# Optimization experiments

Measured on AMD Instinct MI355X. Metric: run time of the kernel, lower is better.

The kernel has to match this reference:

```python
import jax, jax.numpy as jnp
import numpy as np

N_HEADS = 16
LATENT = 16          # latent_vec_len (1D RoPE portion of head_dim)
ROPE_BASE = 10000.0
HIDDEN = 1024


def _rope_1d_tables(seq_len, d):
    m = d // 2
    inv_freq = 1.0 / (ROPE_BASE ** (jnp.arange(m, dtype=jnp.float32) * 2.0 / d))
    ang = jnp.arange(seq_len, dtype=jnp.float32)[:, None] * inv_freq[None, :]  # (S, m)
    return jnp.cos(ang), jnp.sin(ang)


def _rope_2d_tables(height, width, d):
    m = d // 4
    inv_freq = 1.0 / (ROPE_BASE ** (jnp.arange(m, dtype=jnp.float32) * 4.0 / d))
    xa = jnp.arange(width, dtype=jnp.float32)[:, None] * inv_freq[None, :]   # (W, m)
    ya = jnp.arange(height, dtype=jnp.float32)[:, None] * inv_freq[None, :]  # (H, m)
    S = height * width
    cos_x = jnp.broadcast_to(jnp.cos(xa)[None, :, :], (height, width, m)).reshape(S, m)
    sin_x = jnp.broadcast_to(jnp.sin(xa)[None, :, :], (height, width, m)).reshape(S, m)
    cos_y = jnp.broadcast_to(jnp.cos(ya)[:, None, :], (height, width, m)).reshape(S, m)
    sin_y = jnp.broadcast_to(jnp.sin(ya)[:, None, :], (height, width, m)).reshape(S, m)
    return cos_x, sin_x, cos_y, sin_y


def _apply_rope_1d(x, cos, sin):
    # x: (B, n, S, d) with d even; cos/sin: (S, d//2)
    d = x.shape[-1]
    xr = x.reshape(*x.shape[:-1], d // 2, 2)
    a, b = xr[..., 0], xr[..., 1]
    na = a * cos - b * sin
    nb = a * sin + b * cos
    return jnp.stack((na, nb), axis=-1).reshape(x.shape)


def _apply_rope_2d(x, cos_x, sin_x, cos_y, sin_y):
    # x: (B, n, S, d) with d % 4 == 0; tables: (S, d//4)
    q = x.shape[-1] // 4
    xr, xi = x[..., :q], x[..., q:2 * q]
    yr, yi = x[..., 2 * q:3 * q], x[..., 3 * q:]
    return jnp.concatenate([
        xr * cos_x - xi * sin_x,
        xr * sin_x + xi * cos_x,
        yr * cos_y - yi * sin_y,
        yr * sin_y + yi * cos_y,
    ], axis=-1)


def setup_inputs() -> dict:
    key = jax.random.key(0)
    ks = jax.random.split(key, 9)
    B, S, D = 16, 1024, HIDDEN
    s = 1.0 / np.sqrt(D)
    inp = {
        'x': jax.random.normal(ks[0], (B, S, D), dtype=jnp.float32),
        'Wq': jax.random.uniform(ks[1], (D, D), jnp.float32, -s, s),
        'bq': jax.random.uniform(ks[2], (D,), jnp.float32, -s, s),
        'Wk': jax.random.uniform(ks[3], (D, D), jnp.float32, -s, s),
        'bk': jax.random.uniform(ks[4], (D,), jnp.float32, -s, s),
        'Wv': jax.random.uniform(ks[5], (D, D), jnp.float32, -s, s),
        'bv': jax.random.uniform(ks[6], (D,), jnp.float32, -s, s),
        'Wo': jax.random.uniform(ks[7], (D, D), jnp.float32, -s, s),
        'bo': jax.random.uniform(ks[8], (D,), jnp.float32, -s, s),
        'height': 32,
        'width': 32,
    }
    return inp


def reference(x, Wq, bq, Wk, bk, Wv, bv, Wo, bo, height, width):
    B, S, D = x.shape
    n, h = N_HEADS, D // N_HEADS
    spatial = h - LATENT
    scale = 1.0 / np.sqrt(h)

    def heads(t):
        return t.reshape(B, S, n, h).transpose(0, 2, 1, 3)  # (B, n, S, h)

    q = heads(x @ Wq.T + bq)
    k = heads(x @ Wk.T + bk)
    v = heads(x @ Wv.T + bv)

    cos1, sin1 = _rope_1d_tables(S, LATENT)
    cx, sx, cy, sy = _rope_2d_tables(height, width, spatial)

    ql = _apply_rope_1d(q[..., :LATENT], cos1, sin1)
    kl = _apply_rope_1d(k[..., :LATENT], cos1, sin1)
    qs = _apply_rope_2d(q[..., LATENT:], cx, sx, cy, sy)
    ks_ = _apply_rope_2d(k[..., LATENT:], cx, sx, cy, sy)

    qr = jnp.concatenate([ql, qs], axis=-1)
    kr = jnp.concatenate([kl, ks_], axis=-1)

    attn = jax.nn.softmax(jnp.einsum('bnsh,bnth->bnst', qr, kr) * scale, axis=-1)
    out = jnp.einsum('bnst,bnth->bnsh', attn, v)
    out = out.transpose(0, 2, 1, 3).reshape(B, S, D)
    return out @ Wo.T + bo
```

## Files before the change

### kernel.cpp

```cpp
#include <hip/hip_runtime.h>
#include <math.h>

#define B_ 16
#define S_ 1024
#define D_ 1024
#define NH_ 16
#define M_TOT (B_ * S_)

typedef __attribute__((ext_vector_type(8))) short short8v;
typedef __attribute__((ext_vector_type(4))) short short4v;
typedef __attribute__((ext_vector_type(4))) float float4v;
typedef __attribute__((ext_vector_type(4))) unsigned int uint4v;

static __device__ __forceinline__ unsigned short f2bf(float f) {
  union { float f; unsigned u; } x; x.f = f;
  unsigned r = (x.u + 0x7fffu + ((x.u >> 16) & 1u)) >> 16;
  return (unsigned short)r;
}
static __device__ __forceinline__ float bf2f(unsigned short u) {
  union { unsigned u; float f; } x; x.u = ((unsigned)u) << 16;
  return x.f;
}

static __device__ __forceinline__ unsigned pack2bf(float a, float b) {
  return ((unsigned)f2bf(b) << 16) | (unsigned)f2bf(a);
}

static __device__ __forceinline__ void load_lds16(const unsigned short* g, unsigned short* l) {
  __builtin_amdgcn_global_load_lds(
      (const __attribute__((address_space(1))) unsigned int*)g,
      (__attribute__((address_space(3))) unsigned int*)l, 16, 0, 0);
}

__global__ __launch_bounds__(256) void prep(
    const float* __restrict__ x, unsigned short* __restrict__ xb,
    const float* __restrict__ w0, const float* __restrict__ w1,
    const float* __restrict__ w2, const float* __restrict__ w3,
    unsigned short* __restrict__ wdst,
    float* __restrict__ cos1, float* __restrict__ sin1,
    float* __restrict__ cos2, float* __restrict__ sin2) {
  const int bid = blockIdx.x;
  if (bid < 16384) {
    int i = bid * 256 + threadIdx.x;
    float4 v = ((const float4*)x)[i];
    unsigned short tt[4] = {f2bf(v.x), f2bf(v.y), f2bf(v.z), f2bf(v.w)};
    ((short4v*)xb)[i] = *(short4v*)tt;
  } else if (bid < 20480) {
    int wi = (bid - 16384) * 256 + threadIdx.x;
    int m = wi >> 18;
    int i = wi & 262143;
    const float* src = (m == 0) ? w0 : (m == 1) ? w1 : (m == 2) ? w2 : w3;
    float4 v = ((const float4*)src)[i];
    unsigned short tt[4] = {f2bf(v.x), f2bf(v.y), f2bf(v.z), f2bf(v.w)};
    ((short4v*)(wdst + (size_t)m * D_ * D_))[i] = *(short4v*)tt;
  } else {
    int t = (bid - 20480) * 256 + threadIdx.x;
    if (t < S_ * 8) {
      int s = t >> 3, i = t & 7;
      double ang = (double)s * pow(10000.0, -(double)i / 8.0);
      cos1[t] = (float)cos(ang);
      sin1[t] = (float)sin(ang);
    } else if (t < S_ * 8 + 384) {
      int u = t - S_ * 8;
      int p = u / 12, j = u - p * 12;
      double ang = (double)p * pow(10000.0, -(double)j / 12.0);
      cos2[u] = (float)cos(ang);
      sin2[u] = (float)sin(ang);
    }
  }
}

template <bool BF16OUT>
__global__ __launch_bounds__(256) void gemm_mfma(
    const unsigned short* __restrict__ A, const unsigned short* __restrict__ Wall,
    const float* __restrict__ b0, const float* __restrict__ b1,
    const float* __restrict__ b2, void* __restrict__ Cout) {
  __shared__ unsigned short As[2][128 * 32];
  __shared__ unsigned short Bs[2][128 * 32];
  const int y = blockIdx.y;
  const unsigned short* W = Wall + (size_t)y * D_ * D_;
  const float* bias = (y == 0) ? b0 : (y == 1) ? b1 : b2;
  const int t = threadIdx.x;
  const int w = t >> 6, L = t & 63;
  const int c = L & 15, g = L >> 4;
  const int id = blockIdx.x;
  const int xcd = id & 7, slot = id >> 3;
  const int bn = (slot & 7) * 128;
  const int bm = ((slot >> 3) * 8 + xcd) * 128;

  const int srow = w * 32 + (L >> 2);
  const int sko = (L & 3) * 8;
  const unsigned short* gA = A + (size_t)(bm + srow) * D_ + sko;
  const unsigned short* gB = W + (size_t)(bn + srow) * D_ + sko;

  const int wm = (w >> 1) * 64, wn = (w & 1) * 64;

  float4v acc[4][4];
#pragma unroll
  for (int i = 0; i < 4; ++i)
#pragma unroll
    for (int j = 0; j < 4; ++j) acc[i][j] = (float4v){0.f, 0.f, 0.f, 0.f};

#define GS(buf, k0_)                                                  \
  {                                                                   \
    load_lds16(gA + (k0_), &As[buf][w * 1024]);                       \
    load_lds16(gA + (k0_) + 16 * D_, &As[buf][w * 1024 + 512]);       \
    load_lds16(gB + (k0_), &Bs[buf][w * 1024]);                       \
    load_lds16(gB + (k0_) + 16 * D_, &Bs[buf][w * 1024 + 512]);       \
  }

  GS(0, 0);
  asm volatile("s_waitcnt vmcnt(0)" ::: "memory");
  __syncthreads();
  int cur = 0;
  for (int k0 = 0; k0 < D_; k0 += 32) {
    if (k0 + 32 < D_) GS(cur ^ 1, k0 + 32);
    short8v af[4], bf[4];
#pragma unroll
    for (int i = 0; i < 4; ++i)
      af[i] = *(const short8v*)&As[cur][(wm + 16 * i + c) * 32 + 8 * g];
#pragma unroll
    for (int j = 0; j < 4; ++j)
      bf[j] = *(const short8v*)&Bs[cur][(wn + 16 * j + c) * 32 + 8 * g];
#pragma unroll
    for (int i = 0; i < 4; ++i)
#pragma unroll
      for (int j = 0; j < 4; ++j)
        acc[i][j] = __builtin_amdgcn_mfma_f32_16x16x32_bf16(af[i], bf[j], acc[i][j], 0, 0, 0);
    asm volatile("s_waitcnt vmcnt(0)" ::: "memory");
    __syncthreads();
    cur ^= 1;
  }
#undef GS
  unsigned short* Cb = (unsigned short*)Cout + (size_t)y * M_TOT * D_;
#pragma unroll
  for (int i = 0; i < 4; ++i)
#pragma unroll
    for (int r = 0; r < 4; ++r) {
      const size_t row = (size_t)bm + wm + 16 * i + 4 * g + r;
#pragma unroll
      for (int j = 0; j < 4; ++j) {
        const int col = bn + wn + 16 * j + c;
        float vv = acc[i][j][r] + bias[col];
        if (BF16OUT)
          Cb[row * D_ + col] = f2bf(vv);
        else
          ((float*)Cout)[row * D_ + col] = vv;
      }
    }
}

__global__ __launch_bounds__(256) void postproc(
    unsigned short* __restrict__ qb, unsigned short* __restrict__ kbuf,
    const unsigned short* __restrict__ vb, unsigned short* __restrict__ vT,
    const float* __restrict__ cos1, const float* __restrict__ sin1,
    const float* __restrict__ cos2, const float* __restrict__ sin2) {
  __shared__ unsigned short T[64][72];
  const int bid = blockIdx.x;
  if (bid < 65536) {
    unsigned short* q = (bid < 32768) ? qb : kbuf;
    const float scale = (bid < 32768) ? 0.125f : 1.0f;
    int tid = (bid & 32767) * 256 + threadIdx.x;
    int u = tid & 511;
    int m = tid >> 9;
    int s = m & (S_ - 1);
    int head = u >> 5, w = u & 31;
    size_t base = (size_t)m * D_ + head * 64;
    size_t c0, c1;
    float cv, sv;
    if (w < 8) {
      c0 = base + 2 * w; c1 = c0 + 1;
      cv = cos1[s * 8 + w]; sv = sin1[s * 8 + w];
    } else if (w < 20) {
      int j = w - 8, x = s & 31;
      c0 = base + 16 + j; c1 = base + 28 + j;
      cv = cos2[x * 12 + j]; sv = sin2[x * 12 + j];
    } else {
      int j = w - 20, yy = s >> 5;
      c0 = base + 40 + j; c1 = base + 52 + j;
      cv = cos2[yy * 12 + j]; sv = sin2[yy * 12 + j];
    }
    float a = bf2f(q[c0]), b = bf2f(q[c1]);
    q[c0] = f2bf((a * cv - b * sv) * scale);
    q[c1] = f2bf((a * sv + b * cv) * scale);
  } else {
    const int tb = bid - 65536;
    const int t = threadIdx.x;
    const int st0 = (tb & 15) * 64;
    const int hd = (tb >> 4) & 15, b = tb >> 8;
    const unsigned short* src = vb + ((size_t)b * S_ + st0) * D_ + hd * 64;
#pragma unroll
    for (int rep = 0; rep < 4; ++rep) {
      int id = t + rep * 256;
      int s = id >> 4, n4 = (id & 15) * 4;
      short4v val = *(const short4v*)(src + (size_t)s * D_ + n4);
      T[n4 + 0][s] = val[0]; T[n4 + 1][s] = val[1];
      T[n4 + 2][s] = val[2]; T[n4 + 3][s] = val[3];
    }
    __syncthreads();
    unsigned short* dst = vT + ((size_t)(b * NH_ + hd) * 64) * S_ + st0;
#pragma unroll
    for (int rep = 0; rep < 2; ++rep) {
      int id = t + rep * 256;
      int n = id >> 3, s8 = (id & 7) * 8;
      unsigned short tmp[8];
#pragma unroll
      for (int u2 = 0; u2 < 8; ++u2) tmp[u2] = T[n][s8 + u2];
      *(short8v*)(dst + (size_t)n * S_ + s8) = *(short8v*)tmp;
    }
  }
}

__global__ __launch_bounds__(256, 4) void attn_mfma(
    const unsigned short* __restrict__ qb, const unsigned short* __restrict__ kb,
    const unsigned short* __restrict__ vT, unsigned short* __restrict__ out) {
  __shared__ unsigned short KV[2][2][4096];
  const int t = threadIdx.x;
  const int w = t >> 6;
  const int L = t & 63;
  const int c = L & 15;
  const int g = L >> 4;
  const int id = blockIdx.x;
  const int xcd = id & 7, slot = id >> 3;
  const int qt = slot & 7;
  const int pair = (slot >> 3) * 8 + xcd;
  const int b = pair >> 4, hd = pair & 15;
  const size_t mrow0 = (size_t)b * S_ + qt * 128 + w * 32;
  const int dcol0 = hd * 64;

  const int lrow = L >> 3;
  const int lcol = ((L & 7) ^ lrow) * 8;

  const int a_lo = (((L & 16) ? 32 : 0) + c) * 4;
  const int a_hi = a_lo + 64;
  const bool ghi = (L >= 32);
  const int swz = (c & 7) << 3;

  short8v aq[2][2];
#pragma unroll
  for (int i = 0; i < 2; ++i)
#pragma unroll
    for (int st = 0; st < 2; ++st)
      aq[i][st] = *(const short8v*)(qb + (mrow0 + 16 * i + c) * D_ + dcol0 + 32 * st + 8 * g);

  float4v oacc[2][4];
  float lsum[2] = {0.f, 0.f};
#pragma unroll
  for (int i = 0; i < 2; ++i)
#pragma unroll
    for (int jv = 0; jv < 4; ++jv) oacc[i][jv] = (float4v){0.f, 0.f, 0.f, 0.f};

  const unsigned short* vbase = vT + (size_t)(b * NH_ + hd) * 64 * S_;
  const unsigned short* kbb = kb + (size_t)b * S_ * D_ + dcol0;

#define STAGE(buf, kt_)                                                          \
  {                                                                              \
    _Pragma("unroll")                                                            \
    for (int e = 0; e < 2; ++e) {                                                \
      const int seg = 2 * w + e;                                                 \
      const int row = seg * 8 + lrow;                                            \
      load_lds16(kbb + (size_t)((kt_) * 64 + row) * D_ + lcol,                   \
                 &KV[buf][0][seg * 512]);                                        \
      load_lds16(vbase + (size_t)row * S_ + (kt_) * 64 + lcol,                   \
                 &KV[buf][1][seg * 512]);                                        \
    }                                                                            \
  }

  STAGE(0, 0);
  asm volatile("s_waitcnt vmcnt(0)" ::: "memory");
  __syncthreads();

#pragma unroll 1
  for (int kt = 0; kt < 16; ++kt) {
    const int cur = kt & 1;
    if (kt < 15) STAGE(cur ^ 1, kt + 1);
#pragma unroll
    for (int st = 0; st < 2; ++st) {
      short8v vfh[4];
#pragma unroll
      for (int jv = 0; jv < 4; ++jv)
        vfh[jv] = *(const short8v*)&KV[cur][1][((16 * jv + c) * 64 + st * 32 + 8 * g) ^ swz];
      short8v kfh[2][2];
#pragma unroll
      for (int jl = 0; jl < 2; ++jl)
#pragma unroll
        for (int h = 0; h < 2; ++h)
          kfh[jl][h] = *(const short8v*)&KV[cur][0][((16 * (2 * st + jl) + c) * 64 + h * 32 + 8 * g) ^ swz];
      float4v sacch[2][2];
#pragma unroll
      for (int i = 0; i < 2; ++i)
#pragma unroll
        for (int jl = 0; jl < 2; ++jl) sacch[i][jl] = (float4v){0.f, 0.f, 0.f, 0.f};
      __builtin_amdgcn_s_setprio(1);
#pragma unroll
      for (int jl = 0; jl < 2; ++jl)
#pragma unroll
        for (int i = 0; i < 2; ++i) {
          sacch[i][jl] = __builtin_amdgcn_mfma_f32_16x16x32_bf16(kfh[jl][0], aq[i][0], sacch[i][jl], 0, 0, 0);
          sacch[i][jl] = __builtin_amdgcn_mfma_f32_16x16x32_bf16(kfh[jl][1], aq[i][1], sacch[i][jl], 0, 0, 0);
        }
      __builtin_amdgcn_s_setprio(0);
      unsigned pkh[2][2][2];
#pragma unroll
      for (int i = 0; i < 2; ++i)
#pragma unroll
        for (int jl = 0; jl < 2; ++jl) {
          float p0 = __expf(sacch[i][jl][0]);
          float p1 = __expf(sacch[i][jl][1]);
          float p2 = __expf(sacch[i][jl][2]);
          float p3 = __expf(sacch[i][jl][3]);
          lsum[i] += (p0 + p1) + (p2 + p3);
          pkh[i][jl][0] = pack2bf(p0, p1);
          pkh[i][jl][1] = pack2bf(p2, p3);
        }
      short8v aph[2];
#pragma unroll
      for (int i = 0; i < 2; ++i) {
        uint4v wv;
#pragma unroll
        for (int q2 = 0; q2 < 4; ++q2) {
          const int addr = (q2 & 2) ? a_hi : a_lo;
          int vlo = __builtin_amdgcn_ds_bpermute(addr, (int)pkh[i][0][q2 & 1]);
          int vhi = __builtin_amdgcn_ds_bpermute(addr, (int)pkh[i][1][q2 & 1]);
          wv[q2] = (unsigned)(ghi ? vhi : vlo);
        }
        aph[i] = *(short8v*)&wv;
      }
      __builtin_amdgcn_s_setprio(1);
#pragma unroll
      for (int jv = 0; jv < 4; ++jv)
#pragma unroll
        for (int i = 0; i < 2; ++i)
          oacc[i][jv] = __builtin_amdgcn_mfma_f32_16x16x32_bf16(aph[i], vfh[jv], oacc[i][jv], 0, 0, 0);
      __builtin_amdgcn_s_setprio(0);
    }
    asm volatile("s_waitcnt vmcnt(0)" ::: "memory");
    __syncthreads();
  }
#undef STAGE
#pragma unroll
  for (int i = 0; i < 2; ++i) {
    float ls = lsum[i];
    ls += __shfl_xor(ls, 16);
    ls += __shfl_xor(ls, 32);
#pragma unroll
    for (int r = 0; r < 4; ++r) {
      float inv = 1.f / __shfl(ls, 4 * g + r);
      size_t row = mrow0 + 16 * i + 4 * g + r;
#pragma unroll
      for (int jv = 0; jv < 4; ++jv)
        out[row * D_ + dcol0 + 16 * jv + c] = f2bf(oacc[i][jv][r] * inv);
    }
  }
}

extern "C" void kernel_launch(void* const* d_in, const int* in_sizes, int n_in,
                              void* d_out, int out_size, void* d_ws, size_t ws_size,
                              hipStream_t stream) {
  const float* x  = (const float*)d_in[0];
  const float* Wq = (const float*)d_in[1];
  const float* bq = (const float*)d_in[2];
  const float* Wk = (const float*)d_in[3];
  const float* bk = (const float*)d_in[4];
  const float* Wv = (const float*)d_in[5];
  const float* bv = (const float*)d_in[6];
  const float* Wo = (const float*)d_in[7];
  const float* bo = (const float*)d_in[8];
  float* out = (float*)d_out;

  char* ws = (char*)d_ws;
  const size_t SZ2 = (size_t)M_TOT * D_ * 2;
  unsigned short* xb = (unsigned short*)(ws);
  unsigned short* ob = xb;
  unsigned short* qb = (unsigned short*)(ws + SZ2);
  unsigned short* kb = (unsigned short*)(ws + 2 * SZ2);
  unsigned short* vb = (unsigned short*)(ws + 3 * SZ2);
  unsigned short* vT = (unsigned short*)(ws + 4 * SZ2);
  unsigned short* wqb = (unsigned short*)(ws + 5 * SZ2);
  unsigned short* wob = wqb + 3 * (size_t)D_ * D_;
  float* cos1 = (float*)(ws + 5 * SZ2 + 4 * (size_t)D_ * D_ * 2);
  float* sin1 = cos1 + S_ * 8;
  float* cos2 = sin1 + S_ * 8;
  float* sin2 = cos2 + 384;

  prep<<<20514, 256, 0, stream>>>(x, xb, Wq, Wk, Wv, Wo, wqb,
                                  cos1, sin1, cos2, sin2);
  gemm_mfma<true><<<dim3(1024, 3), 256, 0, stream>>>(xb, wqb, bq, bk, bv, qb);
  postproc<<<69632, 256, 0, stream>>>(qb, kb, vb, vT, cos1, sin1, cos2, sin2);
  attn_mfma<<<2048, 256, 0, stream>>>(qb, kb, vT, ob);
  gemm_mfma<false><<<dim3(1024, 1), 256, 0, stream>>>(ob, wob, bo, bo, bo, out);
}
```

Baseline: 485.4 us.

## Triple-buffer GEMM LDS tiles with partial vmcnt waits and single barrier

Switches the projection GEMM from double to triple-buffered LDS staging. Each step waits only for the older tile's loads (vmcnt(4)) and issues one raw s_barrier before prefetching two tiles ahead. The aim is to keep global-to-LDS loads in flight across MFMA compute instead of draining every iteration. It costs 50% more LDS per block, which may reduce occupancy, and the hand-counted wait/barrier ordering must be correct to avoid races.

After: 466.7 us. 3.8% less time.

```diff
diff --git a/kernel.cpp b/kernel.cpp
--- a/kernel.cpp
+++ b/kernel.cpp
@@ -75,8 +75,8 @@
     const unsigned short* __restrict__ A, const unsigned short* __restrict__ Wall,
     const float* __restrict__ b0, const float* __restrict__ b1,
     const float* __restrict__ b2, void* __restrict__ Cout) {
-  __shared__ unsigned short As[2][128 * 32];
-  __shared__ unsigned short Bs[2][128 * 32];
+  __shared__ unsigned short As[3][128 * 32];
+  __shared__ unsigned short Bs[3][128 * 32];
   const int y = blockIdx.y;
   const unsigned short* W = Wall + (size_t)y * D_ * D_;
   const float* bias = (y == 0) ? b0 : (y == 1) ? b1 : b2;
@@ -101,37 +101,48 @@
 #pragma unroll
     for (int j = 0; j < 4; ++j) acc[i][j] = (float4v){0.f, 0.f, 0.f, 0.f};
 
-#define GS(buf, k0_)                                                  \
-  {                                                                   \
-    load_lds16(gA + (k0_), &As[buf][w * 1024]);                       \
-    load_lds16(gA + (k0_) + 16 * D_, &As[buf][w * 1024 + 512]);       \
-    load_lds16(gB + (k0_), &Bs[buf][w * 1024]);                       \
-    load_lds16(gB + (k0_) + 16 * D_, &Bs[buf][w * 1024 + 512]);       \
+#define GS(buf, kt_)                                                   \
+  {                                                                    \
+    load_lds16(gA + (kt_) * 32, &As[buf][w * 1024]);                   \
+    load_lds16(gA + (kt_) * 32 + 16 * D_, &As[buf][w * 1024 + 512]);   \
+    load_lds16(gB + (kt_) * 32, &Bs[buf][w * 1024]);                   \
+    load_lds16(gB + (kt_) * 32 + 16 * D_, &Bs[buf][w * 1024 + 512]);   \
+  }
+#define VWAIT4 asm volatile("s_waitcnt vmcnt(4)" ::: "memory")
+#define VWAIT0 asm volatile("s_waitcnt vmcnt(0)" ::: "memory")
+#define BARRIER asm volatile("s_barrier" ::: "memory")
+#define COMPUTE(cur)                                                     \
+  {                                                                      \
+    short8v af[4], bf[4];                                                \
+    _Pragma("unroll")                                                    \
+    for (int i = 0; i < 4; ++i)                                          \
+      af[i] = *(const short8v*)&As[cur][(wm + 16 * i + c) * 32 + 8 * g]; \
+    _Pragma("unroll")                                                    \
+    for (int j = 0; j < 4; ++j)                                          \
+      bf[j] = *(const short8v*)&Bs[cur][(wn + 16 * j + c) * 32 + 8 * g]; \
+    _Pragma("unroll")                                                    \
+    for (int i = 0; i < 4; ++i)                                          \
+      _Pragma("unroll")                                                  \
+      for (int j = 0; j < 4; ++j)                                        \
+        acc[i][j] = __builtin_amdgcn_mfma_f32_16x16x32_bf16(             \
+            af[i], bf[j], acc[i][j], 0, 0, 0);                           \
   }
 
   GS(0, 0);
-  asm volatile("s_waitcnt vmcnt(0)" ::: "memory");
-  __syncthreads();
-  int cur = 0;
-  for (int k0 = 0; k0 < D_; k0 += 32) {
-    if (k0 + 32 < D_) GS(cur ^ 1, k0 + 32);
-    short8v af[4], bf[4];
-#pragma unroll
-    for (int i = 0; i < 4; ++i)
-      af[i] = *(const short8v*)&As[cur][(wm + 16 * i + c) * 32 + 8 * g];
-#pragma unroll
-    for (int j = 0; j < 4; ++j)
-      bf[j] = *(const short8v*)&Bs[cur][(wn + 16 * j + c) * 32 + 8 * g];
-#pragma unroll
-    for (int i = 0; i < 4; ++i)
-#pragma unroll
-      for (int j = 0; j < 4; ++j)
-        acc[i][j] = __builtin_amdgcn_mfma_f32_16x16x32_bf16(af[i], bf[j], acc[i][j], 0, 0, 0);
-    asm volatile("s_waitcnt vmcnt(0)" ::: "memory");
-    __syncthreads();
-    cur ^= 1;
-  }
+  GS(1, 1);
+#pragma unroll 1
+  for (int s = 0; s < 30; s += 3) {
+    VWAIT4; BARRIER; GS(2, s + 2); COMPUTE(0);
+    VWAIT4; BARRIER; GS(0, s + 3); COMPUTE(1);
+    VWAIT4; BARRIER; GS(1, s + 4); COMPUTE(2);
+  }
+  VWAIT4; BARRIER; COMPUTE(0);
+  VWAIT0; BARRIER; COMPUTE(1);
 #undef GS
+#undef VWAIT4
+#undef VWAIT0
+#undef BARRIER
+#undef COMPUTE
   unsigned short* Cb = (unsigned short*)Cout + (size_t)y * M_TOT * D_;
 #pragma unroll
   for (int i = 0; i < 4; ++i)
```
